# Kernel tuning notes

Hardware: AMD Instinct MI355X
Metric: run time of the kernel (lower is better)

The kernel has to match this reference:

```python
import jax, jax.numpy as jnp
import numpy as np

N_QUBITS = 12
DIM = 2 ** N_QUBITS  # 4096

_H = (jnp.array([[1.0, 1.0], [1.0, -1.0]]) / np.sqrt(2.0)).astype(jnp.complex64)
_X = jnp.array([[0.0, 1.0], [1.0, 0.0]], dtype=jnp.complex64)


def setup_inputs() -> dict:
    key = jax.random.key(0)
    k1, k2 = jax.random.split(key)
    state = jax.random.normal(k1, (8, 512, DIM), dtype=jnp.float32)
    params = jax.random.normal(k2, (N_QUBITS,), dtype=jnp.float32)
    return {"state": state, "params": params}


def _to_quantum(x):
    # faithful to _classical_to_quantum_inspired: normalize, phase = acos(|v|), sign * exp(i*phase)
    norms = jnp.linalg.norm(x, axis=-1, keepdims=True)
    v = x / (norms + 1e-8)
    mag = jnp.minimum(jnp.abs(v), 1.0)
    q = (jnp.sign(v) * jnp.exp(1j * jnp.arccos(mag))).astype(jnp.complex64)
    nrm = jnp.sqrt(jnp.sum(q.real ** 2 + q.imag ** 2, axis=-1, keepdims=True))
    return q / nrm.astype(jnp.complex64)


def _axis(q):
    # qubit q = bit q (LSB); tensor axes ordered MSB-first after batch axis 0
    return 1 + (N_QUBITS - 1 - q)


def _apply_1q(full, q, U):
    ax = _axis(q)
    moved = jnp.moveaxis(full, ax, -1)
    out = jnp.einsum('...b,ab->...a', moved, U)
    return jnp.moveaxis(out, -1, ax)


def _apply_ctrl(full, c, t, U):
    # apply U on target qubit t where control qubit c == 1
    axc = _axis(c)
    b0 = jnp.take(full, 0, axis=axc)
    b1 = jnp.take(full, 1, axis=axc)
    axt = _axis(t)
    axt_sub = axt - 1 if axt > axc else axt
    moved = jnp.moveaxis(b1, axt_sub, -1)
    b1n = jnp.moveaxis(jnp.einsum('...b,ab->...a', moved, U), -1, axt_sub)
    return jnp.stack([b0, b1n], axis=axc)


def _rx(theta):
    c = jnp.cos(theta / 2).astype(jnp.complex64)
    s = (-1j * jnp.sin(theta / 2)).astype(jnp.complex64)
    return jnp.stack([jnp.stack([c, s]), jnp.stack([s, c])])


def reference(state, params):
    B, T, D = state.shape
    psi = _to_quantum(state.reshape(B * T, D))  # (N, 2**n) complex64
    full = psi.reshape((B * T,) + (2,) * N_QUBITS)
    for q in range(N_QUBITS):
        full = _apply_1q(full, q, _H)                                  # Hadamard
        full = _apply_ctrl(full, q, (q + 1) % N_QUBITS, _rx(params[q]))  # controlled-RX
        if q < N_QUBITS - 1:
            full = _apply_ctrl(full, q, q + 1, _X)                     # CNOT
    amp = full.reshape(B * T, D)
    probs = amp.real ** 2 + amp.imag ** 2  # measurement probabilities
    return probs.reshape(B, T, D).astype(jnp.float32)
```

## Files before the change

kernel.cpp:

```cpp
#include <hip/hip_runtime.h>

#define NQ  12
#define DIM 4096
#define TPB 256

typedef float v2f __attribute__((ext_vector_type(2)));

__device__ __forceinline__ int SW4(int i) { return i ^ ((i >> 4) & 31); }
__device__ __forceinline__ int SW5(int i) { return i ^ ((i >> 5) & 31); }

__device__ __forceinline__ float wave_reduce(float v) {
#pragma unroll
    for (int m = 32; m >= 1; m >>= 1) v += __shfl_xor(v, m, 64);
    return v;
}

#define BCAST(v, q) __uint_as_float(__builtin_amdgcn_readlane(__float_as_uint(v), (q)))

template <int MC, int MT, bool XGATE>
__device__ __forceinline__ void apply_layer(v2f* a, v2f ctv, v2f snv) {
#pragma unroll
    for (int i = 0; i < 16; ++i) {
        if (i & MC) continue;
        const int j = i | MC;
        const v2f t0 = a[i], t1 = a[j];
        a[i] = t0 + t1;
        a[j] = t0 - t1;
    }
#pragma unroll
    for (int i = 0; i < 16; ++i) {
        if (!(i & MC) || (i & MT)) continue;
        const int j = i | MT;
        const v2f b0 = a[i], b1 = a[j];
        const v2f s0 = snv * b0.yx;
        const v2f s1 = snv * b1.yx;
        if (XGATE) {
            a[i] = ctv * b1 + s0;
            a[j] = ctv * b0 + s1;
        } else {
            a[i] = ctv * b0 + s1;
            a[j] = ctv * b1 + s0;
        }
    }
}

__global__ __launch_bounds__(TPB) void qlayer_kernel(
        const float* __restrict__ state, const float* __restrict__ params,
        float* __restrict__ out) {
    __shared__ float sre[DIM];
    __shared__ float sim[DIM];

    const int t = threadIdx.x;
    const int lane = t & 63;
    const long long sbase = (long long)blockIdx.x * DIM;

    const float th = params[lane < NQ ? lane : 0] * 0.5f;
    const float cl = cosf(th);
    const float sl = sinf(th);

    float x[16];
    const float4* gp = (const float4*)(state + sbase + t * 16);
    float ss = 0.f;
#pragma unroll
    for (int j = 0; j < 4; ++j) {
        const float4 v = gp[j];
        x[4 * j + 0] = v.x; x[4 * j + 1] = v.y;
        x[4 * j + 2] = v.z; x[4 * j + 3] = v.w;
        ss = fmaf(v.x, v.x, ss); ss = fmaf(v.y, v.y, ss);
        ss = fmaf(v.z, v.z, ss); ss = fmaf(v.w, v.w, ss);
    }
    ss = wave_reduce(ss);
    if (lane == 0) sre[t >> 6] = ss;
    __syncthreads();
    const float nrm  = sqrtf(sre[0] + sre[1] + sre[2] + sre[3]);
    const float invd = 1.0f / (nrm + 1e-8f);
    __syncthreads();

    v2f a[16];
#pragma unroll
    for (int k = 0; k < 16; ++k) {
        const float v   = x[k] * invd;
        const float re  = fminf(fmaxf(v, -1.0f), 1.0f);
        const float imb = sqrtf(fmaxf(1.0f - re * re, 0.f));
        const float im  = (v > 0.f) ? imb : ((v < 0.f) ? -imb : 0.f);
        v2f q; q.x = re; q.y = im;
        a[k] = q;
    }

#define CTV(q) ({ v2f _c; _c.x = BCAST(cl, q); _c.y = _c.x; _c; })
#define SNV(q) ({ float _s = BCAST(sl, q); v2f _v; _v.x = _s; _v.y = -_s; _v; })

    apply_layer<1, 2, true>(a, CTV(0), SNV(0));
    apply_layer<2, 4, true>(a, CTV(1), SNV(1));
    apply_layer<4, 8, true>(a, CTV(2), SNV(2));
#pragma unroll
    for (int r = 0; r < 16; ++r) {
        const int s = SW4(t * 16 + r);
        sre[s] = a[r].x; sim[s] = a[r].y;
    }
    __syncthreads();

    {
        const int base = (t & 7) | ((t >> 3) << 7);
        int sa[16];
#pragma unroll
        for (int r = 0; r < 16; ++r) {
            sa[r] = SW4(base | (r << 3));
            v2f q; q.x = sre[sa[r]]; q.y = sim[sa[r]];
            a[r] = q;
        }
        apply_layer<1, 2, true>(a, CTV(3), SNV(3));
        apply_layer<2, 4, true>(a, CTV(4), SNV(4));
        apply_layer<4, 8, true>(a, CTV(5), SNV(5));
#pragma unroll
        for (int r = 0; r < 16; ++r) {
            sre[sa[r]] = a[r].x; sim[sa[r]] = a[r].y;
        }
    }
    __syncthreads();

    {
        const int base = (t & 63) | ((t >> 6) << 10);
#pragma unroll
        for (int r = 0; r < 16; ++r) {
            const int s = SW4(base | (r << 6));
            v2f q; q.x = sre[s]; q.y = sim[s];
            a[r] = q;
        }
        apply_layer<1, 2, true>(a, CTV(6), SNV(6));
        apply_layer<2, 4, true>(a, CTV(7), SNV(7));
        apply_layer<4, 8, true>(a, CTV(8), SNV(8));
#pragma unroll
        for (int r = 0; r < 16; ++r) {
            const int s = SW5(base | (r << 6));
            sre[s] = a[r].x; sim[s] = a[r].y;
        }
    }
    __syncthreads();

    {
        const int base = t << 1;
#pragma unroll
        for (int r = 0; r < 16; ++r) {
            const int s = SW5(base | ((r & 7) << 9) | (r >> 3));
            v2f q; q.x = sre[s]; q.y = sim[s];
            a[r] = q;
        }
        apply_layer<1, 2, true >(a, CTV(9),  SNV(9));
        apply_layer<2, 4, true >(a, CTV(10), SNV(10));
        apply_layer<4, 8, false>(a, CTV(11), SNV(11));

        const float scale = 0x1p-24f;
        float2* outp = (float2*)(out + sbase);
#pragma unroll
        for (int r = 0; r < 8; ++r) {
            const int idx = base | ((r & 7) << 9);
            const v2f q0 = a[r] * a[r];
            const v2f q1 = a[r | 8] * a[r | 8];
            outp[idx >> 1] = make_float2((q0.x + q0.y) * scale,
                                         (q1.x + q1.y) * scale);
        }
    }
#undef CTV
#undef SNV
}

extern "C" void kernel_launch(void* const* d_in, const int* in_sizes, int n_in,
                              void* d_out, int out_size, void* d_ws, size_t ws_size,
                              hipStream_t stream) {
    (void)in_sizes; (void)n_in; (void)out_size; (void)d_ws; (void)ws_size;
    const float* state  = (const float*)d_in[0];
    const float* params = (const float*)d_in[1];
    float* out = (float*)d_out;
    qlayer_kernel<<<dim3(4096), dim3(TPB), 0, stream>>>(state, params, out);
}
```

Before: 126.9 us.

## Store amplitudes as interleaved complex pairs with padded LDS layout and vector accesses

```diff
diff --git a/kernel.cpp b/kernel.cpp
--- a/kernel.cpp
+++ b/kernel.cpp
@@ -5,9 +5,8 @@
 #define TPB 256
 
 typedef float v2f __attribute__((ext_vector_type(2)));
+typedef float v4f __attribute__((ext_vector_type(4)));
 
-__device__ __forceinline__ int SW4(int i) { return i ^ ((i >> 4) & 31); }
-__device__ __forceinline__ int SW5(int i) { return i ^ ((i >> 5) & 31); }
 
 __device__ __forceinline__ float wave_reduce(float v) {
 #pragma unroll
@@ -44,11 +43,11 @@
     }
 }
 
-__global__ __launch_bounds__(TPB) void qlayer_kernel(
+__global__ __launch_bounds__(TPB, 4) void qlayer_kernel(
         const float* __restrict__ state, const float* __restrict__ params,
         float* __restrict__ out) {
-    __shared__ float sre[DIM];
-    __shared__ float sim[DIM];
+    __shared__ __align__(16) v2f amp[DIM + 256];
+    __shared__ float red[4];
 
     const int t = threadIdx.x;
     const int lane = t & 63;
@@ -70,11 +69,10 @@
         ss = fmaf(v.z, v.z, ss); ss = fmaf(v.w, v.w, ss);
     }
     ss = wave_reduce(ss);
-    if (lane == 0) sre[t >> 6] = ss;
+    if (lane == 0) red[t >> 6] = ss;
     __syncthreads();
-    const float nrm  = sqrtf(sre[0] + sre[1] + sre[2] + sre[3]);
+    const float nrm  = sqrtf(red[0] + red[1] + red[2] + red[3]);
     const float invd = 1.0f / (nrm + 1e-8f);
-    __syncthreads();
 
     v2f a[16];
 #pragma unroll
@@ -93,58 +91,54 @@
     apply_layer<1, 2, true>(a, CTV(0), SNV(0));
     apply_layer<2, 4, true>(a, CTV(1), SNV(1));
     apply_layer<4, 8, true>(a, CTV(2), SNV(2));
+    {
+        const int p1base = 16 * t + 2 * (t >> 1);
 #pragma unroll
-    for (int r = 0; r < 16; ++r) {
-        const int s = SW4(t * 16 + r);
-        sre[s] = a[r].x; sim[s] = a[r].y;
-    }
-    __syncthreads();
-
-    {
-        const int base = (t & 7) | ((t >> 3) << 7);
-        int sa[16];
-#pragma unroll
-        for (int r = 0; r < 16; ++r) {
-            sa[r] = SW4(base | (r << 3));
-            v2f q; q.x = sre[sa[r]]; q.y = sim[sa[r]];
-            a[r] = q;
-        }
-        apply_layer<1, 2, true>(a, CTV(3), SNV(3));
-        apply_layer<2, 4, true>(a, CTV(4), SNV(4));
-        apply_layer<4, 8, true>(a, CTV(5), SNV(5));
-#pragma unroll
-        for (int r = 0; r < 16; ++r) {
-            sre[sa[r]] = a[r].x; sim[sa[r]] = a[r].y;
+        for (int k = 0; k < 8; ++k) {
+            v4f w; w.x = a[2 * k].x; w.y = a[2 * k].y;
+            w.z = a[2 * k + 1].x; w.w = a[2 * k + 1].y;
+            *(v4f*)&amp[p1base + 2 * k] = w;
         }
     }
     __syncthreads();
 
     {
-        const int base = (t & 63) | ((t >> 6) << 10);
+        const int p2base = (t & 7) + 136 * (t >> 3);
 #pragma unroll
-        for (int r = 0; r < 16; ++r) {
-            const int s = SW4(base | (r << 6));
-            v2f q; q.x = sre[s]; q.y = sim[s];
-            a[r] = q;
-        }
+        for (int r = 0; r < 16; ++r)
+            a[r] = amp[p2base + 8 * r + 2 * (r >> 2)];
+        apply_layer<1, 2, true>(a, CTV(3), SNV(3));
+        apply_layer<2, 4, true>(a, CTV(4), SNV(4));
+        apply_layer<4, 8, true>(a, CTV(5), SNV(5));
+#pragma unroll
+        for (int r = 0; r < 16; ++r)
+            amp[p2base + 8 * r + 2 * (r >> 2)] = a[r];
+    }
+    __syncthreads();
+
+    {
+        const int p3base = (t & 63) + 2 * ((t & 63) >> 5) + 1088 * (t >> 6);
+#pragma unroll
+        for (int r = 0; r < 16; ++r)
+            a[r] = amp[p3base + 68 * r];
         apply_layer<1, 2, true>(a, CTV(6), SNV(6));
         apply_layer<2, 4, true>(a, CTV(7), SNV(7));
         apply_layer<4, 8, true>(a, CTV(8), SNV(8));
 #pragma unroll
-        for (int r = 0; r < 16; ++r) {
-            const int s = SW5(base | (r << 6));
-            sre[s] = a[r].x; sim[s] = a[r].y;
-        }
+        for (int r = 0; r < 16; ++r)
+            amp[p3base + 68 * r] = a[r];
     }
     __syncthreads();
 
     {
-        const int base = t << 1;
+        const int p4base = 2 * t + 2 * (t >> 4);
 #pragma unroll
-        for (int r = 0; r < 16; ++r) {
-            const int s = SW5(base | ((r & 7) << 9) | (r >> 3));
-            v2f q; q.x = sre[s]; q.y = sim[s];
-            a[r] = q;
+        for (int k = 0; k < 8; ++k) {
+            const v4f v = *(const v4f*)&amp[p4base + 544 * k];
+            v2f q0; q0.x = v.x; q0.y = v.y;
+            v2f q1; q1.x = v.z; q1.y = v.w;
+            a[k] = q0;
+            a[k + 8] = q1;
         }
         apply_layer<1, 2, true >(a, CTV(9),  SNV(9));
         apply_layer<2, 4, true >(a, CTV(10), SNV(10));
@@ -153,12 +147,11 @@
         const float scale = 0x1p-24f;
         float2* outp = (float2*)(out + sbase);
 #pragma unroll
-        for (int r = 0; r < 8; ++r) {
-            const int idx = base | ((r & 7) << 9);
-            const v2f q0 = a[r] * a[r];
-            const v2f q1 = a[r | 8] * a[r | 8];
-            outp[idx >> 1] = make_float2((q0.x + q0.y) * scale,
-                                         (q1.x + q1.y) * scale);
+        for (int k = 0; k < 8; ++k) {
+            const v2f q0 = a[k] * a[k];
+            const v2f q1 = a[k | 8] * a[k | 8];
+            outp[t + (k << 8)] = make_float2((q0.x + q0.y) * scale,
+                                             (q1.x + q1.y) * scale);
         }
     }
 #undef CTV
```

Measured after the change: 121.3 us. 4.4% less time.
